# Performance work log

Hardware: AMD Instinct MI355X
Metric: run time of the kernel (lower is better)

## Reference

```python
import jax, jax.numpy as jnp
import numpy as np

EMBED = 1024
HEADS = 16
HEAD_DIM = EMBED // HEADS
N, S = 2, 2048


def setup_inputs() -> dict:
    key = jax.random.key(0)
    ks = jax.random.split(key, 8)
    scale_p = 1.0 / np.sqrt(HEAD_DIM)
    return {
        "queries": jax.random.normal(ks[0], (N, S, EMBED), jnp.float32),
        "keys": jax.random.normal(ks[1], (N, S, EMBED), jnp.float32),
        "values": jax.random.normal(ks[2], (N, S, EMBED), jnp.float32),
        # per-head projection weights, torch Linear convention: y = x @ W.T
        "Wq": jax.random.normal(ks[3], (HEAD_DIM, HEAD_DIM), jnp.float32) * scale_p,
        "Wk": jax.random.normal(ks[4], (HEAD_DIM, HEAD_DIM), jnp.float32) * scale_p,
        "Wv": jax.random.normal(ks[5], (HEAD_DIM, HEAD_DIM), jnp.float32) * scale_p,
        "Wo": jax.random.normal(ks[6], (EMBED, EMBED), jnp.float32) * (1.0 / np.sqrt(EMBED)),
        "bo": jax.random.normal(ks[7], (EMBED,), jnp.float32) * 0.01,
    }


def reference(queries, keys, values, Wq, Wk, Wv, Wo, bo):
    n, sq, e = queries.shape
    sk = keys.shape[1]
    # split heads: (N, S, H, D)
    q = queries.reshape(n, sq, HEADS, HEAD_DIM)
    k = keys.reshape(n, sk, HEADS, HEAD_DIM)
    v = values.reshape(n, sk, HEADS, HEAD_DIM)
    # per-head linear projections (weights shared across heads), torch Linear: x @ W.T
    q = jnp.einsum('nshd,ed->nshe', q, Wq)
    k = jnp.einsum('nshd,ed->nshe', k, Wk)
    v = jnp.einsum('nshd,ed->nshe', v, Wv)
    # attention scores (N, H, Q, K); NOTE: scaled by sqrt(embed_size), as in source
    energy = jnp.einsum('nqhd,nkhd->nhqk', q, k)
    attention = jax.nn.softmax(energy / jnp.sqrt(jnp.float32(EMBED)), axis=3)
    out = jnp.einsum('nhql,nlhd->nqhd', attention, v).reshape(n, sq, EMBED)
    return out @ Wo.T + bo
```

## Files before the change

### kernel.cpp

```cpp
#include <hip/hip_runtime.h>
#include <hip/hip_bf16.h>

#define NB 2
#define SS 2048
#define EE 1024
#define HH 16
#define DD 64
#define NHD (NB*HH)
#define KT 64

#define QSCALE 0.04508422002777998f

typedef _Float16 half8 __attribute__((ext_vector_type(8)));
typedef _Float16 half4 __attribute__((ext_vector_type(4)));
typedef float floatx4 __attribute__((ext_vector_type(4)));

__device__ __forceinline__ half8 cvt8(const float* p) {
    float4 x = *(const float4*)p;
    float4 y = *(const float4*)(p + 4);
    half8 h = { (_Float16)x.x, (_Float16)x.y, (_Float16)x.z, (_Float16)x.w,
                (_Float16)y.x, (_Float16)y.y, (_Float16)y.z, (_Float16)y.w };
    return h;
}

__device__ __forceinline__ unsigned int pkrtz_u32(float a, float b) {
    return __builtin_bit_cast(unsigned int, __builtin_amdgcn_cvt_pkrtz(a, b));
}

__device__ __forceinline__ int swz64(int row, int colh) {
    return (row << 6) + ((((colh >> 3) ^ (row & 7)) << 3) | (colh & 7));
}

__global__ __launch_bounds__(256) void proj_kernel(
    const float* __restrict__ Q, const float* __restrict__ K, const float* __restrict__ V,
    const float* __restrict__ Wq, const float* __restrict__ Wk, const float* __restrict__ Wv,
    _Float16* __restrict__ Qp, _Float16* __restrict__ Kp, _Float16* __restrict__ Vt)
{
    int t = threadIdx.x, lane = t & 63, wid = t >> 6;
    int lr = lane & 15, lg = lane >> 4;
    int b = blockIdx.x;
    int nh = b >> 5, st = b & 31;
    int n = nh >> 4, h = nh & 15;

    __shared__ __align__(16) _Float16 vt[DD][72];

    const size_t xoff = ((size_t)n * SS + st * 64 + wid * 16 + lr) * EE
                        + (size_t)h * DD + lg * 8;
    const size_t qob = ((size_t)nh * SS + st * 64 + wid * 16 + lg * 4) * DD;

    const float* tens[3] = {Q, K, V};
    const float* wts[3]  = {Wq, Wk, Wv};

    #pragma unroll
    for (int x = 0; x < 3; ++x) {
        const float* Xr = tens[x] + xoff;
        half8 a0 = cvt8(Xr);
        half8 a1 = cvt8(Xr + 32);
        floatx4 acc[4];
        #pragma unroll
        for (int ns = 0; ns < 4; ++ns) {
            const float* Wr = wts[x] + (size_t)(ns * 16 + lr) * DD + lg * 8;
            half8 b0 = cvt8(Wr);
            half8 b1 = cvt8(Wr + 32);
            floatx4 c = (floatx4){0.f, 0.f, 0.f, 0.f};
            c = __builtin_amdgcn_mfma_f32_16x16x32_f16(a0, b0, c, 0, 0, 0);
            c = __builtin_amdgcn_mfma_f32_16x16x32_f16(a1, b1, c, 0, 0, 0);
            acc[ns] = c;
        }
        if (x == 0) {
            #pragma unroll
            for (int ns = 0; ns < 4; ++ns)
                #pragma unroll
                for (int r = 0; r < 4; ++r)
                    Qp[qob + (size_t)r * DD + ns * 16 + lr] = (_Float16)(acc[ns][r] * QSCALE);
        } else if (x == 1) {
            #pragma unroll
            for (int ns = 0; ns < 4; ++ns)
                #pragma unroll
                for (int r = 0; r < 4; ++r)
                    Kp[qob + (size_t)r * DD + ns * 16 + lr] = (_Float16)acc[ns][r];
        } else {
            #pragma unroll
            for (int ns = 0; ns < 4; ++ns)
                #pragma unroll
                for (int r = 0; r < 4; ++r)
                    vt[ns * 16 + lr][wid * 16 + lg * 4 + r] = (_Float16)acc[ns][r];
        }
    }
    __syncthreads();
    {
        int d = t >> 2, q4 = (t & 3) * 16;
        _Float16* dst = Vt + ((size_t)nh * DD + d) * SS + st * 64 + q4;
        *(half8*)dst       = *(const half8*)(&vt[d][q4]);
        *(half8*)(dst + 8) = *(const half8*)(&vt[d][q4 + 8]);
    }
}

__global__ __launch_bounds__(256, 4) void attn_kernel(
    const _Float16* __restrict__ Qp, const _Float16* __restrict__ Kp,
    const _Float16* __restrict__ Vt, _Float16* __restrict__ Of)
{
    int b = blockIdx.x;
    int slot = b >> 3;
    int nh = (b & 7) * 4 + (slot & 3);
    int qt = slot >> 2;
    int n = nh >> 4, h = nh & 15;
    int t = threadIdx.x;
    int lane = t & 63, wid = t >> 6;
    int lr = lane & 15;
    int lg = lane >> 4;

    __shared__ __align__(16) _Float16 kbuf[2][KT * DD];
    __shared__ __align__(16) _Float16 vbuf[2][DD * KT];
    __shared__ __align__(16) _Float16 plds[4][16 * 64];

    const _Float16* Qb = Qp + ((size_t)nh * SS + qt * 64 + wid * 16) * DD;
    const _Float16* Kb = Kp + (size_t)nh * SS * DD;
    const _Float16* Vb = Vt + (size_t)nh * DD * SS;

    half8 qf0 = *(const half8*)(Qb + (size_t)lr * DD + lg * 8);
    half8 qf1 = *(const half8*)(Qb + (size_t)lr * DD + 32 + lg * 8);

    half8 ones = { (_Float16)1.f, (_Float16)1.f, (_Float16)1.f, (_Float16)1.f,
                   (_Float16)1.f, (_Float16)1.f, (_Float16)1.f, (_Float16)1.f };

    int sr = t >> 3, sc = (t & 7) * 8;

    {
        half8 k0 = *(const half8*)(Kb + (size_t)sr * DD + sc);
        half8 k1 = *(const half8*)(Kb + (size_t)(sr + 32) * DD + sc);
        half8 v0 = *(const half8*)(Vb + (size_t)sr * SS + sc);
        half8 v1 = *(const half8*)(Vb + (size_t)(sr + 32) * SS + sc);
        *(half8*)(&kbuf[0][swz64(sr, sc)]) = k0;
        *(half8*)(&kbuf[0][swz64(sr + 32, sc)]) = k1;
        *(half8*)(&vbuf[0][swz64(sr, sc)]) = v0;
        *(half8*)(&vbuf[0][swz64(sr + 32, sc)]) = v1;
    }
    __syncthreads();

    floatx4 oacc[4];
    #pragma unroll
    for (int ns = 0; ns < 4; ++ns) oacc[ns] = (floatx4){0.f, 0.f, 0.f, 0.f};
    floatx4 sacc = (floatx4){0.f, 0.f, 0.f, 0.f};

    int p = 0;
    for (int kb = 0; kb < SS; kb += KT, p ^= 1) {
        int kn = (kb + KT) & (SS - 1);
        half8 sk0 = *(const half8*)(Kb + (size_t)(kn + sr) * DD + sc);
        half8 sk1 = *(const half8*)(Kb + (size_t)(kn + sr + 32) * DD + sc);
        half8 sv0 = *(const half8*)(Vb + (size_t)sr * SS + kn + sc);
        half8 sv1 = *(const half8*)(Vb + (size_t)(sr + 32) * SS + kn + sc);

        half8 kf[4][2];
        #pragma unroll
        for (int ns = 0; ns < 4; ++ns) {
            kf[ns][0] = *(const half8*)(&kbuf[p][swz64(ns * 16 + lr, lg * 8)]);
            kf[ns][1] = *(const half8*)(&kbuf[p][swz64(ns * 16 + lr, 32 + lg * 8)]);
        }
        floatx4 sc_[4];
        #pragma unroll
        for (int ns = 0; ns < 4; ++ns) {
            floatx4 c = (floatx4){0.f, 0.f, 0.f, 0.f};
            c = __builtin_amdgcn_mfma_f32_16x16x32_f16(kf[ns][0], qf0, c, 0, 0, 0);
            c = __builtin_amdgcn_mfma_f32_16x16x32_f16(kf[ns][1], qf1, c, 0, 0, 0);
            sc_[ns] = c;
        }
        half8 vf[4][2];
        #pragma unroll
        for (int ns = 0; ns < 4; ++ns) {
            vf[ns][0] = *(const half8*)(&vbuf[p][swz64(ns * 16 + lr, lg * 8)]);
            vf[ns][1] = *(const half8*)(&vbuf[p][swz64(ns * 16 + lr, 32 + lg * 8)]);
        }
        #pragma unroll
        for (int ns = 0; ns < 4; ++ns) {
            float p0 = exp2f(fminf(sc_[ns][0], 50.f));
            float p1 = exp2f(fminf(sc_[ns][1], 50.f));
            float p2 = exp2f(fminf(sc_[ns][2], 50.f));
            float p3 = exp2f(fminf(sc_[ns][3], 50.f));
            uint2 pr;
            pr.x = pkrtz_u32(p0, p1);
            pr.y = pkrtz_u32(p2, p3);
            *(uint2*)(&plds[wid][swz64(lr, ns * 16 + lg * 4)]) = pr;
        }
        asm volatile("s_waitcnt lgkmcnt(0)" ::: "memory");
        half8 pf0 = *(const half8*)(&plds[wid][swz64(lr, lg * 8)]);
        half8 pf1 = *(const half8*)(&plds[wid][swz64(lr, 32 + lg * 8)]);
        #pragma unroll
        for (int ns = 0; ns < 4; ++ns) {
            oacc[ns] = __builtin_amdgcn_mfma_f32_16x16x32_f16(pf0, vf[ns][0], oacc[ns], 0, 0, 0);
            oacc[ns] = __builtin_amdgcn_mfma_f32_16x16x32_f16(pf1, vf[ns][1], oacc[ns], 0, 0, 0);
        }
        sacc = __builtin_amdgcn_mfma_f32_16x16x32_f16(pf0, ones, sacc, 0, 0, 0);
        sacc = __builtin_amdgcn_mfma_f32_16x16x32_f16(pf1, ones, sacc, 0, 0, 0);
        *(half8*)(&kbuf[p ^ 1][swz64(sr, sc)]) = sk0;
        *(half8*)(&kbuf[p ^ 1][swz64(sr + 32, sc)]) = sk1;
        *(half8*)(&vbuf[p ^ 1][swz64(sr, sc)]) = sv0;
        *(half8*)(&vbuf[p ^ 1][swz64(sr + 32, sc)]) = sv1;
        __syncthreads();
    }

    float linv[4];
    #pragma unroll
    for (int r = 0; r < 4; ++r)
        linv[r] = 1.f / sacc[r];

    _Float16* Ob = Of + ((size_t)n * SS + qt * 64 + wid * 16) * EE + h * DD;
    #pragma unroll
    for (int ns = 0; ns < 4; ++ns)
        #pragma unroll
        for (int r = 0; r < 4; ++r)
            Ob[(size_t)(lg * 4 + r) * EE + ns * 16 + lr] = (_Float16)(oacc[ns][r] * linv[r]);
}

__global__ __launch_bounds__(256) void wconv_kernel(
    const float* __restrict__ W, _Float16* __restrict__ Wf)
{
    int i = (blockIdx.x * 256 + threadIdx.x) * 8;
    *(half8*)(Wf + i) = cvt8(W + i);
}

__global__ __launch_bounds__(256, 2) void oproj_kernel(
    const _Float16* __restrict__ Of, const _Float16* __restrict__ Wf,
    const float* __restrict__ bo, float* __restrict__ out)
{
    int b = blockIdx.x;
    int mb = b & 63, nb = b >> 6;
    int t = threadIdx.x, lane = t & 63, wid = t >> 6;
    int wm = wid >> 1, wn = wid & 1;
    int lr = lane & 15, lg = lane >> 4;
    int m0 = mb * 64, n0 = nb * 128;

    __shared__ __align__(16) _Float16 As[2][64][72];
    __shared__ __align__(16) _Float16 Bs[2][128][72];

    int arow = t >> 2, acol = (t & 3) * 16;
    int brow = t >> 1, bcol = (t & 1) * 32;
    const _Float16* Ag = Of + (size_t)(m0 + arow) * EE + acol;
    const _Float16* Bg = Wf + (size_t)(n0 + brow) * EE + bcol;

    floatx4 acc[2][4];
    #pragma unroll
    for (int sm = 0; sm < 2; ++sm)
        #pragma unroll
        for (int sn = 0; sn < 4; ++sn) acc[sm][sn] = (floatx4){0.f, 0.f, 0.f, 0.f};

    #pragma unroll
    for (int j = 0; j < 2; ++j)
        *(half8*)(&As[0][arow][acol + j * 8]) = *(const half8*)(Ag + j * 8);
    #pragma unroll
    for (int j = 0; j < 4; ++j)
        *(half8*)(&Bs[0][brow][bcol + j * 8]) = *(const half8*)(Bg + j * 8);
    __syncthreads();

    int p = 0;
    for (int kb = 0; kb < EE; kb += 64, p ^= 1) {
        int kn = kb + 64;
        half8 sa[2], sb[4];
        if (kn < EE) {
            #pragma unroll
            for (int j = 0; j < 2; ++j) sa[j] = *(const half8*)(Ag + kn + j * 8);
            #pragma unroll
            for (int j = 0; j < 4; ++j) sb[j] = *(const half8*)(Bg + kn + j * 8);
        }
        #pragma unroll
        for (int kk = 0; kk < 2; ++kk) {
            half8 af[2], bf[4];
            #pragma unroll
            for (int s = 0; s < 2; ++s)
                af[s] = *(const half8*)(&As[p][wm * 32 + s * 16 + lr][kk * 32 + lg * 8]);
            #pragma unroll
            for (int s = 0; s < 4; ++s)
                bf[s] = *(const half8*)(&Bs[p][wn * 64 + s * 16 + lr][kk * 32 + lg * 8]);
            #pragma unroll
            for (int sm = 0; sm < 2; ++sm)
                #pragma unroll
                for (int sn = 0; sn < 4; ++sn)
                    acc[sm][sn] = __builtin_amdgcn_mfma_f32_16x16x32_f16(
                        af[sm], bf[sn], acc[sm][sn], 0, 0, 0);
        }
        if (kn < EE) {
            #pragma unroll
            for (int j = 0; j < 2; ++j)
                *(half8*)(&As[p ^ 1][arow][acol + j * 8]) = sa[j];
            #pragma unroll
            for (int j = 0; j < 4; ++j)
                *(half8*)(&Bs[p ^ 1][brow][bcol + j * 8]) = sb[j];
        }
        __syncthreads();
    }

    #pragma unroll
    for (int sn = 0; sn < 4; ++sn) {
        int nn = n0 + wn * 64 + sn * 16 + lr;
        float bn = bo[nn];
        #pragma unroll
        for (int sm = 0; sm < 2; ++sm) {
            #pragma unroll
            for (int r = 0; r < 4; ++r)
                out[(size_t)(m0 + wm * 32 + sm * 16 + lg * 4 + r) * EE + nn]
                    = acc[sm][sn][r] + bn;
        }
    }
}

extern "C" void kernel_launch(void* const* d_in, const int* in_sizes, int n_in,
                              void* d_out, int out_size, void* d_ws, size_t ws_size,
                              hipStream_t stream)
{
    const float* Q  = (const float*)d_in[0];
    const float* K  = (const float*)d_in[1];
    const float* V  = (const float*)d_in[2];
    const float* Wq = (const float*)d_in[3];
    const float* Wk = (const float*)d_in[4];
    const float* Wv = (const float*)d_in[5];
    const float* Wo = (const float*)d_in[6];
    const float* bo = (const float*)d_in[7];
    float* out = (float*)d_out;

    const size_t NSE = (size_t)NB * SS * EE;
    _Float16* Qp = (_Float16*)d_ws;
    _Float16* Kp = Qp + NSE;
    _Float16* Vt = Kp + NSE;
    _Float16* Of = Vt + NSE;
    _Float16* Wf = Of + NSE;

    proj_kernel<<<1024, 256, 0, stream>>>(Q, K, V, Wq, Wk, Wv, Qp, Kp, Vt);
    wconv_kernel<<<(EE * EE) / (256 * 8), 256, 0, stream>>>(Wo, Wf);
    attn_kernel<<<NHD * (SS / 64), 256, 0, stream>>>(Qp, Kp, Vt, Of);
    oproj_kernel<<<512, 256, 0, stream>>>(Of, Wf, bo, out);
}
```

Baseline: 207.9 us.

## Fold Wo conversion into projection kernel and interleave QK/exp/PV in attention loop

Result: no change. 206.0 us (-0.9%).

```diff
diff --git a/kernel.cpp b/kernel.cpp
--- a/kernel.cpp
+++ b/kernel.cpp
@@ -34,13 +34,20 @@
 __global__ __launch_bounds__(256) void proj_kernel(
     const float* __restrict__ Q, const float* __restrict__ K, const float* __restrict__ V,
     const float* __restrict__ Wq, const float* __restrict__ Wk, const float* __restrict__ Wv,
-    _Float16* __restrict__ Qp, _Float16* __restrict__ Kp, _Float16* __restrict__ Vt)
+    const float* __restrict__ Wo,
+    _Float16* __restrict__ Qp, _Float16* __restrict__ Kp, _Float16* __restrict__ Vt,
+    _Float16* __restrict__ Wf)
 {
     int t = threadIdx.x, lane = t & 63, wid = t >> 6;
     int lr = lane & 15, lg = lane >> 4;
     int b = blockIdx.x;
     int nh = b >> 5, st = b & 31;
     int n = nh >> 4, h = nh & 15;
+
+    if (t < 128) {
+        int i = b * 1024 + t * 8;
+        *(half8*)(Wf + i) = cvt8(Wo + i);
+    }
 
     __shared__ __align__(16) _Float16 vt[DD][72];
 
@@ -157,41 +164,69 @@
             kf[ns][0] = *(const half8*)(&kbuf[p][swz64(ns * 16 + lr, lg * 8)]);
             kf[ns][1] = *(const half8*)(&kbuf[p][swz64(ns * 16 + lr, 32 + lg * 8)]);
         }
-        floatx4 sc_[4];
-        #pragma unroll
-        for (int ns = 0; ns < 4; ++ns) {
-            floatx4 c = (floatx4){0.f, 0.f, 0.f, 0.f};
-            c = __builtin_amdgcn_mfma_f32_16x16x32_f16(kf[ns][0], qf0, c, 0, 0, 0);
-            c = __builtin_amdgcn_mfma_f32_16x16x32_f16(kf[ns][1], qf1, c, 0, 0, 0);
-            sc_[ns] = c;
-        }
+        floatx4 s0 = (floatx4){0.f, 0.f, 0.f, 0.f};
+        floatx4 s1 = (floatx4){0.f, 0.f, 0.f, 0.f};
+        s0 = __builtin_amdgcn_mfma_f32_16x16x32_f16(kf[0][0], qf0, s0, 0, 0, 0);
+        s0 = __builtin_amdgcn_mfma_f32_16x16x32_f16(kf[0][1], qf1, s0, 0, 0, 0);
+        s1 = __builtin_amdgcn_mfma_f32_16x16x32_f16(kf[1][0], qf0, s1, 0, 0, 0);
+        s1 = __builtin_amdgcn_mfma_f32_16x16x32_f16(kf[1][1], qf1, s1, 0, 0, 0);
+
+        {
+            float p0 = exp2f(fminf(s0[0], 50.f)), p1 = exp2f(fminf(s0[1], 50.f));
+            float p2 = exp2f(fminf(s0[2], 50.f)), p3 = exp2f(fminf(s0[3], 50.f));
+            uint2 pr; pr.x = pkrtz_u32(p0, p1); pr.y = pkrtz_u32(p2, p3);
+            *(uint2*)(&plds[wid][swz64(lr, 0 * 16 + lg * 4)]) = pr;
+        }
+        {
+            float p0 = exp2f(fminf(s1[0], 50.f)), p1 = exp2f(fminf(s1[1], 50.f));
+            float p2 = exp2f(fminf(s1[2], 50.f)), p3 = exp2f(fminf(s1[3], 50.f));
+            uint2 pr; pr.x = pkrtz_u32(p0, p1); pr.y = pkrtz_u32(p2, p3);
+            *(uint2*)(&plds[wid][swz64(lr, 1 * 16 + lg * 4)]) = pr;
+        }
+
+        floatx4 s2 = (floatx4){0.f, 0.f, 0.f, 0.f};
+        floatx4 s3 = (floatx4){0.f, 0.f, 0.f, 0.f};
+        s2 = __builtin_amdgcn_mfma_f32_16x16x32_f16(kf[2][0], qf0, s2, 0, 0, 0);
+        s2 = __builtin_amdgcn_mfma_f32_16x16x32_f16(kf[2][1], qf1, s2, 0, 0, 0);
+        s3 = __builtin_amdgcn_mfma_f32_16x16x32_f16(kf[3][0], qf0, s3, 0, 0, 0);
+        s3 = __builtin_amdgcn_mfma_f32_16x16x32_f16(kf[3][1], qf1, s3, 0, 0, 0);
+
         half8 vf[4][2];
         #pragma unroll
         for (int ns = 0; ns < 4; ++ns) {
             vf[ns][0] = *(const half8*)(&vbuf[p][swz64(ns * 16 + lr, lg * 8)]);
             vf[ns][1] = *(const half8*)(&vbuf[p][swz64(ns * 16 + lr, 32 + lg * 8)]);
         }
-        #pragma unroll
-        for (int ns = 0; ns < 4; ++ns) {
-            float p0 = exp2f(fminf(sc_[ns][0], 50.f));
-            float p1 = exp2f(fminf(sc_[ns][1], 50.f));
-            float p2 = exp2f(fminf(sc_[ns][2], 50.f));
-            float p3 = exp2f(fminf(sc_[ns][3], 50.f));
-            uint2 pr;
-            pr.x = pkrtz_u32(p0, p1);
-            pr.y = pkrtz_u32(p2, p3);
-            *(uint2*)(&plds[wid][swz64(lr, ns * 16 + lg * 4)]) = pr;
-        }
+
         asm volatile("s_waitcnt lgkmcnt(0)" ::: "memory");
         half8 pf0 = *(const half8*)(&plds[wid][swz64(lr, lg * 8)]);
+
+        {
+            float p0 = exp2f(fminf(s2[0], 50.f)), p1 = exp2f(fminf(s2[1], 50.f));
+            float p2 = exp2f(fminf(s2[2], 50.f)), p3 = exp2f(fminf(s2[3], 50.f));
+            uint2 pr; pr.x = pkrtz_u32(p0, p1); pr.y = pkrtz_u32(p2, p3);
+            *(uint2*)(&plds[wid][swz64(lr, 2 * 16 + lg * 4)]) = pr;
+        }
+        {
+            float p0 = exp2f(fminf(s3[0], 50.f)), p1 = exp2f(fminf(s3[1], 50.f));
+            float p2 = exp2f(fminf(s3[2], 50.f)), p3 = exp2f(fminf(s3[3], 50.f));
+            uint2 pr; pr.x = pkrtz_u32(p0, p1); pr.y = pkrtz_u32(p2, p3);
+            *(uint2*)(&plds[wid][swz64(lr, 3 * 16 + lg * 4)]) = pr;
+        }
+
+        #pragma unroll
+        for (int ns = 0; ns < 4; ++ns)
+            oacc[ns] = __builtin_amdgcn_mfma_f32_16x16x32_f16(pf0, vf[ns][0], oacc[ns], 0, 0, 0);
+        sacc = __builtin_amdgcn_mfma_f32_16x16x32_f16(pf0, ones, sacc, 0, 0, 0);
+
+        asm volatile("s_waitcnt lgkmcnt(0)" ::: "memory");
         half8 pf1 = *(const half8*)(&plds[wid][swz64(lr, 32 + lg * 8)]);
-        #pragma unroll
-        for (int ns = 0; ns < 4; ++ns) {
-            oacc[ns] = __builtin_amdgcn_mfma_f32_16x16x32_f16(pf0, vf[ns][0], oacc[ns], 0, 0, 0);
+
+        #pragma unroll
+        for (int ns = 0; ns < 4; ++ns)
             oacc[ns] = __builtin_amdgcn_mfma_f32_16x16x32_f16(pf1, vf[ns][1], oacc[ns], 0, 0, 0);
-        }
-        sacc = __builtin_amdgcn_mfma_f32_16x16x32_f16(pf0, ones, sacc, 0, 0, 0);
         sacc = __builtin_amdgcn_mfma_f32_16x16x32_f16(pf1, ones, sacc, 0, 0, 0);
+
         *(half8*)(&kbuf[p ^ 1][swz64(sr, sc)]) = sk0;
         *(half8*)(&kbuf[p ^ 1][swz64(sr + 32, sc)]) = sk1;
         *(half8*)(&vbuf[p ^ 1][swz64(sr, sc)]) = sv0;
@@ -210,13 +245,6 @@
         #pragma unroll
         for (int r = 0; r < 4; ++r)
             Ob[(size_t)(lg * 4 + r) * EE + ns * 16 + lr] = (_Float16)(oacc[ns][r] * linv[r]);
-}
-
-__global__ __launch_bounds__(256) void wconv_kernel(
-    const float* __restrict__ W, _Float16* __restrict__ Wf)
-{
-    int i = (blockIdx.x * 256 + threadIdx.x) * 8;
-    *(half8*)(Wf + i) = cvt8(W + i);
 }
 
 __global__ __launch_bounds__(256, 2) void oproj_kernel(
@@ -324,8 +352,7 @@
     _Float16* Of = Vt + NSE;
     _Float16* Wf = Of + NSE;
 
-    proj_kernel<<<1024, 256, 0, stream>>>(Q, K, V, Wq, Wk, Wv, Qp, Kp, Vt);
-    wconv_kernel<<<(EE * EE) / (256 * 8), 256, 0, stream>>>(Wo, Wf);
+    proj_kernel<<<1024, 256, 0, stream>>>(Q, K, V, Wq, Wk, Wv, Wo, Qp, Kp, Vt, Wf);
     attn_kernel<<<NHD * (SS / 64), 256, 0, stream>>>(Qp, Kp, Vt, Of);
     oproj_kernel<<<512, 256, 0, stream>>>(Of, Wf, bo, out);
 }
```
